# Optimization experiments

Measured on AMD Instinct MI355X. Metric: run time of the kernel, lower is better.

## Reference

```python
import jax, jax.numpy as jnp
import numpy as np

MAXHD, MAXV, MINA, MAXA, DT = 100.0, 40.0, -6.0, 4.0, 0.1
NVEH, NT, IN_DIM, UNITS = 4096, 1024, 12, 20


def setup_inputs() -> dict:
    key = jax.random.key(0)
    ks = jax.random.split(key, 12)
    leadfol_inputs = jax.random.normal(ks[0], (NVEH, NT, IN_DIM), dtype=jnp.float32)
    init_state = jax.random.normal(ks[1], (NVEH, 2), dtype=jnp.float32)
    hidden_states = jnp.zeros((2, NVEH, UNITS), dtype=jnp.float32)
    s = 0.1
    return {
        "leadfol_inputs": leadfol_inputs,
        "init_state": init_state,
        "hidden_states": hidden_states,
        "kernel": s * jax.random.normal(ks[2], (IN_DIM, 4 * UNITS), dtype=jnp.float32),
        "rkernel": s * jax.random.normal(ks[3], (UNITS, 4 * UNITS), dtype=jnp.float32),
        "bias": jnp.zeros((4 * UNITS,), dtype=jnp.float32),
        "W2": s * jax.random.normal(ks[4], (UNITS, 10), dtype=jnp.float32),
        "b2": jnp.zeros((10,), dtype=jnp.float32),
        "Wlc": s * jax.random.normal(ks[5], (10, 3), dtype=jnp.float32),
        "blc": jnp.zeros((3,), dtype=jnp.float32),
        "W1": s * jax.random.normal(ks[6], (10, 1), dtype=jnp.float32),
        "b1": jnp.zeros((1,), dtype=jnp.float32),
    }


def reference(leadfol_inputs, init_state, hidden_states, kernel, rkernel, bias,
              W2, b2, Wlc, blc, W1, b1):
    # time-major for scan: (nt, nveh, 12)
    xs = jnp.transpose(leadfol_inputs, (1, 0, 2))
    pos0, spd0 = init_state[:, 0], init_state[:, 1]
    h0, c0 = hidden_states[0], hidden_states[1]

    def step(carry, x_t):
        pos, spd, h, c = carry
        lead_hd = (x_t[:, :3] - pos[:, None]) / MAXHD
        fol_hd = (pos[:, None] - x_t[:, 3:6]) / MAXHD
        spds = x_t[:, 6:] / MAXV
        inp = jnp.concatenate([lead_hd, fol_hd, spds], axis=1)  # (nveh, 12)
        inp = jnp.where(jnp.isnan(inp), jnp.ones_like(inp), inp)
        # Keras LSTMCell (inference, no dropout): gate order i, f, g, o
        z = inp @ kernel + h @ rkernel + bias
        i_g, f_g, g_g, o_g = jnp.split(z, 4, axis=1)
        c_new = jax.nn.sigmoid(f_g) * c + jax.nn.sigmoid(i_g) * jnp.tanh(g_g)
        h_new = jax.nn.sigmoid(o_g) * jnp.tanh(c_new)
        x2 = jax.nn.relu(h_new @ W2 + b2)          # (nveh, 10)
        lc = x2 @ Wlc + blc                          # (nveh, 3)
        acc_raw = (x2 @ W1 + b1)[:, 0]               # (nveh,)
        acc = (MAXA - MINA) * acc_raw + MINA
        pos_new = pos + DT * spd
        spd_new = spd + DT * acc
        return (pos_new, spd_new, h_new, c_new), (pos_new, lc)

    (pos_f, spd_f, h_f, c_f), (traj, lc_all) = jax.lax.scan(step, (pos0, spd0, h0, c0), xs)
    pred_traj = jnp.transpose(traj, (1, 0))            # (nveh, nt)
    pred_lc_action = jnp.transpose(lc_all, (1, 0, 2))  # (nveh, nt, 3)
    return pred_traj, pred_lc_action, spd_f, (h_f, c_f)
```

## Files before the change

### kernel.cpp

```cpp
#include <hip/hip_runtime.h>
#include <cstdint>

#define NVEH  4096
#define NT    1024
#define INW   12
#define UNITS 20

typedef float f32x2 __attribute__((ext_vector_type(2)));

#define PIN(v)  asm volatile("" : "+v"(v))

#define PKFMA_LO(acc, w, s2) \
    asm("v_pk_fma_f32 %0, %1, %2, %0 op_sel:[0,0,0] op_sel_hi:[1,0,1]" \
        : "+v"(acc) : "v"(w), "v"(s2))
#define PKFMA_HI(acc, w, s2) \
    asm("v_pk_fma_f32 %0, %1, %2, %0 op_sel:[0,1,0] op_sel_hi:[1,1,1]" \
        : "+v"(acc) : "v"(w), "v"(s2))
#define PKMUL_LO(dst, w, s2) \
    asm("v_pk_mul_f32 %0, %1, %2 op_sel:[0,0] op_sel_hi:[1,0]" \
        : "=v"(dst) : "v"(w), "v"(s2))
#define PKFMA(acc, a, b) \
    asm("v_pk_fma_f32 %0, %1, %2, %0" : "+v"(acc) : "v"(a), "v"(b))

__device__ __forceinline__ float fexp2(float x) { return __builtin_amdgcn_exp2f(x); }
__device__ __forceinline__ float frcp(float x)  { return __builtin_amdgcn_rcpf(x); }

__device__ __forceinline__ void gload_lds16(const float* g, float* l) {
    __builtin_amdgcn_global_load_lds(
        (const __attribute__((address_space(1))) unsigned int*)g,
        (__attribute__((address_space(3))) unsigned int*)l,
        16, 0, 0);
}

__global__ __attribute__((amdgpu_waves_per_eu(2, 2))) __launch_bounds__(64)
void rnncf_kernel(const float* __restrict__ x,
                  const float* __restrict__ init_state,
                  const float* __restrict__ hs,
                  const float* __restrict__ K,
                  const float* __restrict__ R,
                  const float* __restrict__ bias,
                  const float* __restrict__ W2,
                  const float* __restrict__ b2,
                  const float* __restrict__ Wlc,
                  const float* __restrict__ blc,
                  const float* __restrict__ W1,
                  const float* __restrict__ b1,
                  float* __restrict__ out)
{
    const int lane = threadIdx.x;
    const int grp  = lane / 20;
    const int sub  = lane % 20;
    const int veh  = blockIdx.x * 3 + grp;
    const bool active = (grp < 3) && (veh < NVEH);
    const int vs = active ? veh : 0;

    __shared__ __align__(16) float x_lds[8][4][12];
    __shared__ __align__(16) float h_lds[4][20];
    __shared__ __align__(16) float x2_lds[4][12];

    const float L2E = 1.4426950408889634f;
    const float sI = -L2E, sF = -L2E, sG = 2.0f * L2E, sO = -L2E;
    f32x2 K01[12], K23[12], R01[20], R23[20], bz01, bz23, kd01, kd23;
#pragma unroll
    for (int k = 0; k < 12; ++k) {
        float ck = (k < 3) ? 0.01f : (k < 6) ? -0.01f : 0.025f;
        K01[k][0] = sI * ck * K[k * 80 + sub];
        K01[k][1] = sF * ck * K[k * 80 + 20 + sub];
        K23[k][0] = sG * ck * K[k * 80 + 40 + sub];
        K23[k][1] = sO * ck * K[k * 80 + 60 + sub];
    }
    {
        float aI = 0, aF = 0, aG = 0, aO = 0;
        for (int k = 0; k < 6; ++k) {
            float sgn = (k < 3) ? -0.01f : 0.01f;
            aI += sgn * K[k * 80 + sub];
            aF += sgn * K[k * 80 + 20 + sub];
            aG += sgn * K[k * 80 + 40 + sub];
            aO += sgn * K[k * 80 + 60 + sub];
        }
        kd01[0] = sI * aI; kd01[1] = sF * aF;
        kd23[0] = sG * aG; kd23[1] = sO * aO;
    }
    bz01[0] = sI * bias[sub];      bz01[1] = sF * bias[20 + sub];
    bz23[0] = sG * bias[40 + sub]; bz23[1] = sO * bias[60 + sub];
#pragma unroll
    for (int k = 0; k < 20; ++k) {
        R01[k][0] = sI * R[k * 80 + sub];      R01[k][1] = sF * R[k * 80 + 20 + sub];
        R23[k][0] = sG * R[k * 80 + 40 + sub]; R23[k][1] = sO * R[k * 80 + 60 + sub];
    }
    const int mh = (sub < 10) ? sub : 9;
    f32x2 W2p[10];
#pragma unroll
    for (int u = 0; u < 10; ++u) {
        W2p[u][0] = W2[(2 * u) * 10 + mh];
        W2p[u][1] = W2[(2 * u + 1) * 10 + mh];
    }
    float b2s = b2[mh];
    const int jl = (sub < 3) ? sub : 0;
    f32x2 Wlcp[5];
#pragma unroll
    for (int m = 0; m < 5; ++m) {
        Wlcp[m][0] = Wlc[(2 * m) * 3 + jl];
        Wlcp[m][1] = Wlc[(2 * m + 1) * 3 + jl];
    }
    float blcs = blc[jl];
    PIN(bz01); PIN(bz23); PIN(kd01); PIN(kd23);
#pragma unroll
    for (int k = 0; k < 12; ++k) { PIN(K01[k]); PIN(K23[k]); }
#pragma unroll
    for (int k = 0; k < 20; ++k) { PIN(R01[k]); PIN(R23[k]); }
#pragma unroll
    for (int u = 0; u < 10; ++u) PIN(W2p[u]);
#pragma unroll
    for (int m = 0; m < 5; ++m) PIN(Wlcp[m]);
    PIN(b2s); PIN(blcs);

    float pos = init_state[vs * 2 + 0];
    float spd = init_state[vs * 2 + 1];
    float c   = hs[(size_t)NVEH * UNITS + (size_t)vs * UNITS + sub];
    float hnew = hs[(size_t)vs * UNITS + sub];

    const bool stg = (lane < 9);
    int sveh = blockIdx.x * 3 + lane / 3;
    if (sveh > NVEH - 1) sveh = NVEH - 1;
    const float* sgp = x + (size_t)sveh * NT * INW + (lane % 3) * 4;
    if (stg) {
#pragma unroll
        for (int t0 = 0; t0 < 8; ++t0)
            gload_lds16(sgp + (size_t)t0 * INW, &x_lds[t0][0][0]);
    }

    h_lds[grp][sub] = hnew;
    __builtin_amdgcn_wave_barrier();
    f32x2 hrp[10];
#pragma unroll
    for (int q = 0; q < 5; ++q) {
        float4 v = ((const float4*)&h_lds[grp][0])[q];
        hrp[2*q][0]   = v.x; hrp[2*q][1]   = v.y;
        hrp[2*q+1][0] = v.z; hrp[2*q+1][1] = v.w;
    }
    __builtin_amdgcn_wave_barrier();

    asm volatile("s_waitcnt vmcnt(7)" ::: "memory");
    f32x2 zKx01, zKx23, zA01, zA23, zB01, zB23;
    {
        float4 u0 = ((const float4*)&x_lds[0][grp][0])[0];
        float4 u1 = ((const float4*)&x_lds[0][grp][0])[1];
        float4 u2 = ((const float4*)&x_lds[0][grp][0])[2];
        f32x2 xp[6];
        xp[0][0]=u0.x; xp[0][1]=u0.y; xp[1][0]=u0.z; xp[1][1]=u0.w;
        xp[2][0]=u1.x; xp[2][1]=u1.y; xp[3][0]=u1.z; xp[3][1]=u1.w;
        xp[4][0]=u2.x; xp[4][1]=u2.y; xp[5][0]=u2.z; xp[5][1]=u2.w;
        zKx01 = bz01; zKx23 = bz23;
#pragma unroll
        for (int q = 0; q < 6; ++q) {
            PKFMA_LO(zKx01, K01[2*q],   xp[q]);
            PKFMA_LO(zKx23, K23[2*q],   xp[q]);
            PKFMA_HI(zKx01, K01[2*q+1], xp[q]);
            PKFMA_HI(zKx23, K23[2*q+1], xp[q]);
        }
    }
    PKMUL_LO(zA01, R01[0], hrp[0]);
    PKMUL_LO(zA23, R23[0], hrp[0]);
    PKFMA_HI(zA01, R01[1], hrp[0]);
    PKFMA_HI(zA23, R23[1], hrp[0]);
#pragma unroll
    for (int q = 1; q < 5; ++q) {
        PKFMA_LO(zA01, R01[2*q],   hrp[q]);
        PKFMA_LO(zA23, R23[2*q],   hrp[q]);
        PKFMA_HI(zA01, R01[2*q+1], hrp[q]);
        PKFMA_HI(zA23, R23[2*q+1], hrp[q]);
    }
    PKMUL_LO(zB01, R01[10], hrp[5]);
    PKMUL_LO(zB23, R23[10], hrp[5]);
    PKFMA_HI(zB01, R01[11], hrp[5]);
    PKFMA_HI(zB23, R23[11], hrp[5]);
#pragma unroll
    for (int q = 6; q < 10; ++q) {
        PKFMA_LO(zB01, R01[2*q],   hrp[q]);
        PKFMA_LO(zB23, R23[2*q],   hrp[q]);
        PKFMA_HI(zB01, R01[2*q+1], hrp[q]);
        PKFMA_HI(zB23, R23[2*q+1], hrp[q]);
    }

    f32x2 x2p[5];
#pragma unroll
    for (int q = 0; q < 5; ++q) { x2p[q][0] = 0.0f; x2p[q][1] = 0.0f; }
    f32x2 posp; posp[0] = pos; posp[1] = 0.0f;

    float* trajp = out + (size_t)vs * NT;
    float* lcp   = out + (size_t)NVEH * NT + (size_t)vs * NT * 3;

    for (int tb = 0; tb < NT; tb += 4) {
        asm volatile("s_waitcnt vmcnt(3)" ::: "memory");

#pragma unroll
        for (int j = 0; j < 4; ++j) {
            const int t = tb + j;

            if (t > 0) {
                float a0 = b1[0], a1 = 0.0f;
#pragma unroll
                for (int m = 0; m < 5; ++m) {
                    a0 = fmaf(x2p[m][0], W1[2*m],   a0);
                    a1 = fmaf(x2p[m][1], W1[2*m+1], a1);
                }
                float accr = a0 + a1;
                spd = fmaf(0.1f, fmaf(10.0f, accr, -6.0f), spd);
                if (active && sub < 3) {
                    f32x2 lc2; lc2[0] = blcs; lc2[1] = 0.0f;
#pragma unroll
                    for (int m = 0; m < 5; ++m) PKFMA(lc2, x2p[m], Wlcp[m]);
                    lcp[(t - 1) * 3 + sub] = lc2[0] + lc2[1];
                }
            }
            const float pold = pos;
            pos = fmaf(0.1f, spd, pold);
            if (active && sub == 0) trajp[t] = pos;
            posp[0] = pold;

            f32x2 z01 = zKx01, z23 = zKx23;
            PKFMA_LO(z01, kd01, posp);
            PKFMA_LO(z23, kd23, posp);
            z01 = (z01 + zA01) + zB01;
            z23 = (z23 + zA23) + zB23;

            float ig = frcp(1.0f + fexp2(z01[0]));
            float fg = frcp(1.0f + fexp2(z01[1]));
            float gg = 1.0f - 2.0f * frcp(fexp2(z23[0]) + 1.0f);
            float og = frcp(1.0f + fexp2(z23[1]));
            c = fmaf(fg, c, ig * gg);
            float th = 1.0f - 2.0f * frcp(fexp2(2.8853900817779268f * c) + 1.0f);
            hnew = og * th;

            h_lds[grp][sub] = hnew;
#pragma unroll
            for (int q = 0; q < 5; ++q) {
                float4 v = ((const float4*)&h_lds[grp][0])[q];
                hrp[2*q][0]   = v.x; hrp[2*q][1]   = v.y;
                hrp[2*q+1][0] = v.z; hrp[2*q+1][1] = v.w;
            }

            f32x2 xm2; xm2[0] = b2s; xm2[1] = 0.0f;
#pragma unroll
            for (int u = 0; u < 10; ++u) PKFMA(xm2, hrp[u], W2p[u]);
            float xm = fmaxf(xm2[0] + xm2[1], 0.0f);
            if (sub < 10) x2_lds[grp][sub] = xm;
            {
                float4 a = ((const float4*)&x2_lds[grp][0])[0];
                float4 b = ((const float4*)&x2_lds[grp][0])[1];
                float2 e = *((const float2*)&x2_lds[grp][8]);
                x2p[0][0]=a.x; x2p[0][1]=a.y; x2p[1][0]=a.z; x2p[1][1]=a.w;
                x2p[2][0]=b.x; x2p[2][1]=b.y; x2p[3][0]=b.z; x2p[3][1]=b.w;
                x2p[4][0]=e.x; x2p[4][1]=e.y;
            }

            PKMUL_LO(zA01, R01[0], hrp[0]);
            PKMUL_LO(zA23, R23[0], hrp[0]);
            PKFMA_HI(zA01, R01[1], hrp[0]);
            PKFMA_HI(zA23, R23[1], hrp[0]);
#pragma unroll
            for (int q = 1; q < 5; ++q) {
                PKFMA_LO(zA01, R01[2*q],   hrp[q]);
                PKFMA_LO(zA23, R23[2*q],   hrp[q]);
                PKFMA_HI(zA01, R01[2*q+1], hrp[q]);
                PKFMA_HI(zA23, R23[2*q+1], hrp[q]);
            }
            PKMUL_LO(zB01, R01[10], hrp[5]);
            PKMUL_LO(zB23, R23[10], hrp[5]);
            PKFMA_HI(zB01, R01[11], hrp[5]);
            PKFMA_HI(zB23, R23[11], hrp[5]);
#pragma unroll
            for (int q = 6; q < 10; ++q) {
                PKFMA_LO(zB01, R01[2*q],   hrp[q]);
                PKFMA_LO(zB23, R23[2*q],   hrp[q]);
                PKFMA_HI(zB01, R01[2*q+1], hrp[q]);
                PKFMA_HI(zB23, R23[2*q+1], hrp[q]);
            }

            {
                int tn = t + 1; if (tn > NT - 1) tn = NT - 1;
                float4 u0 = ((const float4*)&x_lds[tn & 7][grp][0])[0];
                float4 u1 = ((const float4*)&x_lds[tn & 7][grp][0])[1];
                float4 u2 = ((const float4*)&x_lds[tn & 7][grp][0])[2];
                f32x2 xp[6];
                xp[0][0]=u0.x; xp[0][1]=u0.y; xp[1][0]=u0.z; xp[1][1]=u0.w;
                xp[2][0]=u1.x; xp[2][1]=u1.y; xp[3][0]=u1.z; xp[3][1]=u1.w;
                xp[4][0]=u2.x; xp[4][1]=u2.y; xp[5][0]=u2.z; xp[5][1]=u2.w;
                zKx01 = bz01; zKx23 = bz23;
#pragma unroll
                for (int q = 0; q < 6; ++q) {
                    PKFMA_LO(zKx01, K01[2*q],   xp[q]);
                    PKFMA_LO(zKx23, K23[2*q],   xp[q]);
                    PKFMA_HI(zKx01, K01[2*q+1], xp[q]);
                    PKFMA_HI(zKx23, K23[2*q+1], xp[q]);
                }
            }
        }

        if (stg) {
#pragma unroll
            for (int j = 0; j < 4; ++j) {
                int tt = tb + 8 + j; if (tt > NT - 1) tt = NT - 1;
                gload_lds16(sgp + (size_t)tt * INW, &x_lds[(tb + j) & 7][0][0]);
            }
        }
    }

    {
        float a0 = b1[0], a1 = 0.0f;
#pragma unroll
        for (int m = 0; m < 5; ++m) {
            a0 = fmaf(x2p[m][0], W1[2*m],   a0);
            a1 = fmaf(x2p[m][1], W1[2*m+1], a1);
        }
        float accr = a0 + a1;
        spd = fmaf(0.1f, fmaf(10.0f, accr, -6.0f), spd);
        if (active && sub < 3) {
            f32x2 lc2; lc2[0] = blcs; lc2[1] = 0.0f;
#pragma unroll
            for (int m = 0; m < 5; ++m) PKFMA(lc2, x2p[m], Wlcp[m]);
            lcp[(NT - 1) * 3 + sub] = lc2[0] + lc2[1];
        }
    }

    if (active) {
        float* spdf = out + (size_t)NVEH * NT * 4;
        float* hf   = spdf + NVEH;
        float* cf   = hf + (size_t)NVEH * UNITS;
        if (sub == 0) spdf[veh] = spd;
        hf[(size_t)veh * UNITS + sub] = hnew;
        cf[(size_t)veh * UNITS + sub] = c;
    }
}

extern "C" void kernel_launch(void* const* d_in, const int* in_sizes, int n_in,
                              void* d_out, int out_size, void* d_ws, size_t ws_size,
                              hipStream_t stream) {
    const float* x    = (const float*)d_in[0];
    const float* st0  = (const float*)d_in[1];
    const float* hs   = (const float*)d_in[2];
    const float* K    = (const float*)d_in[3];
    const float* R    = (const float*)d_in[4];
    const float* bias = (const float*)d_in[5];
    const float* W2   = (const float*)d_in[6];
    const float* b2   = (const float*)d_in[7];
    const float* Wlc  = (const float*)d_in[8];
    const float* blc  = (const float*)d_in[9];
    const float* W1   = (const float*)d_in[10];
    const float* b1   = (const float*)d_in[11];
    float* out = (float*)d_out;

    dim3 grid((NVEH + 2) / 3);
    dim3 block(64);
    hipLaunchKernelGGL(rnncf_kernel, grid, block, 0, stream,
                       x, st0, hs, K, R, bias, W2, b2, Wlc, blc, W1, b1, out);
}
```

Measured before the change: 690.3 us.

## Replace LDS-staged input ring with direct per-lane global register prefetch

Removes the async global-to-LDS staging ring for the per-step inputs and the explicit vmcnt waits. Each lane now loads its vehicle's 12 inputs directly from global memory into a two-deep register double buffer, about two steps ahead, and the input projection moves earlier in the step. Trajectory outputs are batched into one float4 store every four steps instead of a scalar store per step. The risk is that all 20 lanes of a group issue redundant global loads, and the compiler may insert conservative waits on these loads right inside the serial recurrence.

```diff
diff --git a/kernel.cpp b/kernel.cpp
--- a/kernel.cpp
+++ b/kernel.cpp
@@ -24,13 +24,6 @@
 
 __device__ __forceinline__ float fexp2(float x) { return __builtin_amdgcn_exp2f(x); }
 __device__ __forceinline__ float frcp(float x)  { return __builtin_amdgcn_rcpf(x); }
-
-__device__ __forceinline__ void gload_lds16(const float* g, float* l) {
-    __builtin_amdgcn_global_load_lds(
-        (const __attribute__((address_space(1))) unsigned int*)g,
-        (__attribute__((address_space(3))) unsigned int*)l,
-        16, 0, 0);
-}
 
 __global__ __attribute__((amdgpu_waves_per_eu(2, 2))) __launch_bounds__(64)
 void rnncf_kernel(const float* __restrict__ x,
@@ -54,7 +47,6 @@
     const bool active = (grp < 3) && (veh < NVEH);
     const int vs = active ? veh : 0;
 
-    __shared__ __align__(16) float x_lds[8][4][12];
     __shared__ __align__(16) float h_lds[4][20];
     __shared__ __align__(16) float x2_lds[4][12];
 
@@ -120,16 +112,6 @@
     float c   = hs[(size_t)NVEH * UNITS + (size_t)vs * UNITS + sub];
     float hnew = hs[(size_t)vs * UNITS + sub];
 
-    const bool stg = (lane < 9);
-    int sveh = blockIdx.x * 3 + lane / 3;
-    if (sveh > NVEH - 1) sveh = NVEH - 1;
-    const float* sgp = x + (size_t)sveh * NT * INW + (lane % 3) * 4;
-    if (stg) {
-#pragma unroll
-        for (int t0 = 0; t0 < 8; ++t0)
-            gload_lds16(sgp + (size_t)t0 * INW, &x_lds[t0][0][0]);
-    }
-
     h_lds[grp][sub] = hnew;
     __builtin_amdgcn_wave_barrier();
     f32x2 hrp[10];
@@ -141,12 +123,17 @@
     }
     __builtin_amdgcn_wave_barrier();
 
-    asm volatile("s_waitcnt vmcnt(7)" ::: "memory");
+    const float4* xg = (const float4*)(x + (size_t)vs * NT * INW);
+    float4 xq[2][3];
+#pragma unroll
+    for (int q = 0; q < 3; ++q) {
+        xq[1][q] = xg[1 * 3 + q];
+        xq[0][q] = xg[2 * 3 + q];
+    }
+
     f32x2 zKx01, zKx23, zA01, zA23, zB01, zB23;
     {
-        float4 u0 = ((const float4*)&x_lds[0][grp][0])[0];
-        float4 u1 = ((const float4*)&x_lds[0][grp][0])[1];
-        float4 u2 = ((const float4*)&x_lds[0][grp][0])[2];
+        float4 u0 = xg[0], u1 = xg[1], u2 = xg[2];
         f32x2 xp[6];
         xp[0][0]=u0.x; xp[0][1]=u0.y; xp[1][0]=u0.z; xp[1][1]=u0.w;
         xp[2][0]=u1.x; xp[2][1]=u1.y; xp[3][0]=u1.z; xp[3][1]=u1.w;
@@ -190,10 +177,9 @@
 
     float* trajp = out + (size_t)vs * NT;
     float* lcp   = out + (size_t)NVEH * NT + (size_t)vs * NT * 3;
+    float tj0, tj1, tj2, tj3;
 
     for (int tb = 0; tb < NT; tb += 4) {
-        asm volatile("s_waitcnt vmcnt(3)" ::: "memory");
-
 #pragma unroll
         for (int j = 0; j < 4; ++j) {
             const int t = tb + j;
@@ -216,7 +202,8 @@
             }
             const float pold = pos;
             pos = fmaf(0.1f, spd, pold);
-            if (active && sub == 0) trajp[t] = pos;
+            if (j == 0) tj0 = pos; else if (j == 1) tj1 = pos;
+            else if (j == 2) tj2 = pos; else tj3 = pos;
             posp[0] = pold;
 
             f32x2 z01 = zKx01, z23 = zKx23;
@@ -239,6 +226,28 @@
                 float4 v = ((const float4*)&h_lds[grp][0])[q];
                 hrp[2*q][0]   = v.x; hrp[2*q][1]   = v.y;
                 hrp[2*q+1][0] = v.z; hrp[2*q+1][1] = v.w;
+            }
+
+            {
+                float4 u0 = xq[(j + 1) & 1][0];
+                float4 u1 = xq[(j + 1) & 1][1];
+                float4 u2 = xq[(j + 1) & 1][2];
+                f32x2 xp[6];
+                xp[0][0]=u0.x; xp[0][1]=u0.y; xp[1][0]=u0.z; xp[1][1]=u0.w;
+                xp[2][0]=u1.x; xp[2][1]=u1.y; xp[3][0]=u1.z; xp[3][1]=u1.w;
+                xp[4][0]=u2.x; xp[4][1]=u2.y; xp[5][0]=u2.z; xp[5][1]=u2.w;
+                zKx01 = bz01; zKx23 = bz23;
+#pragma unroll
+                for (int q = 0; q < 6; ++q) {
+                    PKFMA_LO(zKx01, K01[2*q],   xp[q]);
+                    PKFMA_LO(zKx23, K23[2*q],   xp[q]);
+                    PKFMA_HI(zKx01, K01[2*q+1], xp[q]);
+                    PKFMA_HI(zKx23, K23[2*q+1], xp[q]);
+                }
+                int tt = t + 3; if (tt > NT - 1) tt = NT - 1;
+#pragma unroll
+                for (int q = 0; q < 3; ++q)
+                    xq[(j + 1) & 1][q] = xg[tt * 3 + q];
             }
 
             f32x2 xm2; xm2[0] = b2s; xm2[1] = 0.0f;
@@ -277,33 +286,11 @@
                 PKFMA_HI(zB01, R01[2*q+1], hrp[q]);
                 PKFMA_HI(zB23, R23[2*q+1], hrp[q]);
             }
-
-            {
-                int tn = t + 1; if (tn > NT - 1) tn = NT - 1;
-                float4 u0 = ((const float4*)&x_lds[tn & 7][grp][0])[0];
-                float4 u1 = ((const float4*)&x_lds[tn & 7][grp][0])[1];
-                float4 u2 = ((const float4*)&x_lds[tn & 7][grp][0])[2];
-                f32x2 xp[6];
-                xp[0][0]=u0.x; xp[0][1]=u0.y; xp[1][0]=u0.z; xp[1][1]=u0.w;
-                xp[2][0]=u1.x; xp[2][1]=u1.y; xp[3][0]=u1.z; xp[3][1]=u1.w;
-                xp[4][0]=u2.x; xp[4][1]=u2.y; xp[5][0]=u2.z; xp[5][1]=u2.w;
-                zKx01 = bz01; zKx23 = bz23;
-#pragma unroll
-                for (int q = 0; q < 6; ++q) {
-                    PKFMA_LO(zKx01, K01[2*q],   xp[q]);
-                    PKFMA_LO(zKx23, K23[2*q],   xp[q]);
-                    PKFMA_HI(zKx01, K01[2*q+1], xp[q]);
-                    PKFMA_HI(zKx23, K23[2*q+1], xp[q]);
-                }
-            }
-        }
-
-        if (stg) {
-#pragma unroll
-            for (int j = 0; j < 4; ++j) {
-                int tt = tb + 8 + j; if (tt > NT - 1) tt = NT - 1;
-                gload_lds16(sgp + (size_t)tt * INW, &x_lds[(tb + j) & 7][0][0]);
-            }
+        }
+
+        if (active && sub == 0) {
+            float4 tv; tv.x = tj0; tv.y = tj1; tv.z = tj2; tv.w = tj3;
+            *(float4*)&trajp[tb] = tv;
         }
     }
 
```

After: 1.005 ms. +45.6%, slower.
